# Performance work log

Measured on AMD Instinct MI355X. Metric: run time of the kernel, lower is better.

Reference implementation:

```python
import jax, jax.numpy as jnp
import numpy as np

BITS = 4
PACK = 32 // BITS            # 8 nibbles per int32
IN, OUT = 4096, 4096
NNZ = 75008


def setup_inputs() -> dict:
    key = jax.random.key(0)
    ks = jax.random.split(key, 7)
    x = jax.random.normal(ks[0], (4, 2048, IN), jnp.float32)
    # packed 4-bit indices: any int32 bit pattern is valid after masking
    qweight = jax.random.randint(ks[1], (IN // PACK, OUT), 0, 2147483647, jnp.int32)
    lookup_table = jax.random.normal(ks[2], (OUT, 2 ** BITS), jnp.float32)
    bias = jax.random.normal(ks[3], (OUT,), jnp.float32)
    rows = jnp.sort(jax.random.randint(ks[4], (OUT + 1,), 0, NNZ, jnp.int32))
    outlier_rows = rows.at[0].set(0).at[-1].set(NNZ)  # valid CSR crow
    outlier_cols = jax.random.randint(ks[5], (NNZ,), 0, IN, jnp.int32)
    outlier_vals = jax.random.normal(ks[6], (NNZ,), jnp.float32)
    return {
        'x': x,
        'lookup_table': lookup_table,
        'bias': bias,
        'outlier_vals': outlier_vals,
        'qweight': qweight,
        'outlier_rows': outlier_rows,
        'outlier_cols': outlier_cols,
    }


def _dequant_weight(qweight, lookup_table):
    # unpack 8 4-bit indices per int32 along the packed-infeatures axis
    shifts = (jnp.arange(PACK, dtype=jnp.int32) * BITS)
    idx = ((qweight[:, None, :] >> shifts[None, :, None]) & 0xF)  # [IN//8, 8, OUT]
    idx = idx.reshape(IN, OUT)                                     # [IN, OUT]
    # per-output-channel LUT gather: W[o, i] = lut[o, idx[i, o]]
    return jnp.take_along_axis(lookup_table, idx.T, axis=1)       # [OUT, IN]


def reference(x, lookup_table, bias, outlier_vals, qweight, outlier_rows, outlier_cols):
    W = _dequant_weight(qweight, lookup_table)
    # CSR outlier correction: scatter-add sparse values into the dense weight
    row_ids = jnp.clip(
        jnp.searchsorted(outlier_rows, jnp.arange(NNZ, dtype=jnp.int32), side='right') - 1,
        0, OUT - 1)
    W = W.at[row_ids, outlier_cols].add(outlier_vals)
    x2 = x.reshape(-1, IN)
    y = x2 @ W.T + bias                                            # [B, OUT]
    return y.reshape(x.shape[:-1] + (OUT,))
```

## Files before the change

### kernel.cpp

```cpp
#include <hip/hip_runtime.h>
#include <stdint.h>

#define IN_F  4096
#define OUT_F 4096

typedef unsigned short u16;
typedef __attribute__((ext_vector_type(8))) short bf16x8;
typedef __attribute__((ext_vector_type(4))) float f32x4;

__device__ __forceinline__ u16 f2bf(float f) {
    union { float f; unsigned u; } c; c.f = f;
    unsigned u = c.u;
    return (u16)((u + 0x7FFFu + ((u >> 16) & 1u)) >> 16);
}
__device__ __forceinline__ float bf2f(u16 h) {
    union { unsigned u; float f; } c; c.u = ((unsigned)h) << 16;
    return c.f;
}

__device__ __forceinline__ void load_lds16(const void* g, void* l) {
    unsigned loff = (unsigned)(uintptr_t)l;
    loff = (unsigned)__builtin_amdgcn_readfirstlane((int)loff);
    __builtin_amdgcn_global_load_lds(
        (const __attribute__((address_space(1))) void*)(uintptr_t)g,
        (__attribute__((address_space(3))) void*)(uintptr_t)loff,
        16, 0, 0);
}

#define DQ_O 64
#define DQ_I 256

__global__ __launch_bounds__(256) void dequant_k(const int* __restrict__ qw,
                                                 const float* __restrict__ lut,
                                                 const int* __restrict__ rows,
                                                 const int* __restrict__ cols,
                                                 const float* __restrict__ vals,
                                                 u16* __restrict__ W) {
    __shared__ __align__(16) u16 sW[DQ_O * DQ_I];
    __shared__ u16 slut[DQ_O * 18];

    const int tid = threadIdx.x;
    const int o0 = blockIdx.y * DQ_O;
    const int i0 = blockIdx.x * DQ_I;
    const int p0 = i0 >> 3;

    {
        const int idx = tid * 4;
        const float4 v = *(const float4*)(lut + (size_t)o0 * 16 + idx);
        u16* d = slut + (idx >> 4) * 18 + (idx & 15);
        d[0] = f2bf(v.x); d[1] = f2bf(v.y); d[2] = f2bf(v.z); d[3] = f2bf(v.w);
    }
    __syncthreads();

    const int o_l = tid & 63;
    const int swz = o_l & 31;
#pragma unroll
    for (int it = 0; it < 8; ++it) {
        const int p = (tid >> 6) + it * 4;
        const unsigned w = (unsigned)qw[(size_t)(p0 + p) * OUT_F + (o0 + o_l)];
        union { u16 h[8]; uint4 v; } u;
#pragma unroll
        for (int j = 0; j < 8; ++j)
            u.h[j] = slut[o_l * 18 + ((w >> (4 * j)) & 15u)];
        *(uint4*)(sW + o_l * DQ_I + ((p ^ swz) << 3)) = u.v;
    }
    __syncthreads();

    if (tid < DQ_O) {
        const int s = rows[o0 + tid], e = rows[o0 + tid + 1];
        for (int k = s; k < e; ++k) {
            const unsigned j = (unsigned)(cols[k] - i0);
            if (j < DQ_I) {
                u16* p16 = sW + tid * DQ_I + (((j >> 3) ^ swz) << 3) + (j & 7);
                *p16 = f2bf(bf2f(*p16) + vals[k]);
            }
        }
    }
    __syncthreads();

    const int ch = tid & 31;
#pragma unroll
    for (int it = 0; it < 8; ++it) {
        const int r = (tid >> 5) + it * 8;
        *(uint4*)(W + (size_t)(o0 + r) * IN_F + i0 + ch * 8) =
            *(const uint4*)(sW + r * DQ_I + ((ch ^ (r & 31)) << 3));
    }
}

__global__ __launch_bounds__(256) void cvtx_k(const float4* __restrict__ x,
                                              u16* __restrict__ xb) {
    const size_t i = (size_t)blockIdx.x * 256 + threadIdx.x;
    const float4 a = x[2 * i];
    const float4 b = x[2 * i + 1];
    union { u16 h[8]; uint4 v; } u;
    u.h[0] = f2bf(a.x); u.h[1] = f2bf(a.y); u.h[2] = f2bf(a.z); u.h[3] = f2bf(a.w);
    u.h[4] = f2bf(b.x); u.h[5] = f2bf(b.y); u.h[6] = f2bf(b.z); u.h[7] = f2bf(b.w);
    *(uint4*)(xb + i * 8) = u.v;
}

#define BM 128
#define BN 128
#define BK 32
#define GK 4096

__global__ __launch_bounds__(256) void gemm_k(const u16* __restrict__ A,
                                              const u16* __restrict__ B,
                                              const float* __restrict__ bias,
                                              float* __restrict__ C,
                                              int M, int N) {
    __shared__ __align__(16) u16 sA[BM * BK];
    __shared__ __align__(16) u16 sB[BN * BK];

    const int tid  = threadIdx.x;
    const int wave = tid >> 6;
    const int lane = tid & 63;
    const int bm = blockIdx.y * BM;
    const int bn = blockIdx.x * BN;

    const int srow = wave * 16 + (lane >> 2);
    const int scol = (lane & 3) * 8;

    const u16* ga0 = A + (size_t)(bm + srow) * GK + scol;
    const u16* ga1 = ga0 + (size_t)64 * GK;
    const u16* gb0 = B + (size_t)(bn + srow) * GK + scol;
    const u16* gb1 = gb0 + (size_t)64 * GK;

    u16* la0 = sA + wave * 512;
    u16* la1 = la0 + 2048;
    u16* lb0 = sB + wave * 512;
    u16* lb1 = lb0 + 2048;

    const int frow = lane & 15;
    const int fk   = (lane >> 4) * 8;

    const int wm = (wave >> 1) * 64;
    const int wn = (wave & 1) * 64;

    f32x4 acc[4][4] = {};

    for (int k0 = 0; k0 < GK; k0 += BK) {
        __syncthreads();
        load_lds16(ga0 + k0, la0);
        load_lds16(ga1 + k0, la1);
        load_lds16(gb0 + k0, lb0);
        load_lds16(gb1 + k0, lb1);
        __syncthreads();

        bf16x8 af[4], bfr[4];
#pragma unroll
        for (int t = 0; t < 4; ++t) {
            af[t]  = *(const bf16x8*)(sA + (wm + t * 16 + frow) * BK + fk);
            bfr[t] = *(const bf16x8*)(sB + (wn + t * 16 + frow) * BK + fk);
        }
#pragma unroll
        for (int i = 0; i < 4; ++i)
#pragma unroll
            for (int j = 0; j < 4; ++j)
                acc[i][j] = __builtin_amdgcn_mfma_f32_16x16x32_bf16(
                    af[i], bfr[j], acc[i][j], 0, 0, 0);
    }

    const int cm = bm + wm;
    const int cn = bn + wn;
#pragma unroll
    for (int j = 0; j < 4; ++j) {
        const int col = cn + j * 16 + (lane & 15);
        const float bv = bias[col];
#pragma unroll
        for (int i = 0; i < 4; ++i) {
            const int r0 = cm + i * 16 + (lane >> 4) * 4;
#pragma unroll
            for (int r = 0; r < 4; ++r)
                C[(size_t)(r0 + r) * N + col] = acc[i][j][r] + bv;
        }
    }
}

extern "C" void kernel_launch(void* const* d_in, const int* in_sizes, int n_in,
                              void* d_out, int out_size, void* d_ws, size_t ws_size,
                              hipStream_t stream) {
    (void)n_in; (void)out_size; (void)ws_size;
    const float* x     = (const float*)d_in[0];
    const float* lut   = (const float*)d_in[1];
    const float* bias  = (const float*)d_in[2];
    const float* ovals = (const float*)d_in[3];
    const int*   qw    = (const int*)d_in[4];
    const int*   orows = (const int*)d_in[5];
    const int*   ocols = (const int*)d_in[6];
    float* y = (float*)d_out;

    const int M = in_sizes[0] / IN_F;

    u16* W  = (u16*)d_ws;
    u16* xb = (u16*)((char*)d_ws + (size_t)OUT_F * IN_F * 2);

    dim3 dq_grid(IN_F / DQ_I, OUT_F / DQ_O);
    dequant_k<<<dq_grid, 256, 0, stream>>>(qw, lut, orows, ocols, ovals, W);
    cvtx_k<<<(size_t)M * IN_F / 8 / 256, 256, 0, stream>>>((const float4*)x, xb);
    dim3 grid(OUT_F / BN, M / BM);
    gemm_k<<<grid, 256, 0, stream>>>(xb, W, bias, y, M, OUT_F);
}
```

Before: 562.7 us.

## Fuse fp32-to-bf16 activation conversion into GEMM A-tile loads

Drops the separate cvtx kernel that converted x to a bf16 workspace copy. The GEMM now streams fp32 activation tiles straight into LDS with a rotated column layout, then packs them to bf16 with a perm instruction while building MFMA fragments. This removes one full read and write pass over the activations and one kernel launch. In exchange, each GEMM block moves twice as many A bytes through global/L2 and LDS per k-step, and the rounding changes from round-to-nearest-even to round-half-up.

```diff
diff --git a/kernel.cpp b/kernel.cpp
--- a/kernel.cpp
+++ b/kernel.cpp
@@ -16,6 +16,10 @@
 __device__ __forceinline__ float bf2f(u16 h) {
     union { unsigned u; float f; } c; c.u = ((unsigned)h) << 16;
     return c.f;
+}
+__device__ __forceinline__ unsigned pkbf(float lo, float hi) {
+    union { float f; unsigned u; } a, b; a.f = lo; b.f = hi;
+    return __builtin_amdgcn_perm(b.u + 0x8000u, a.u + 0x8000u, 0x07060302u);
 }
 
 __device__ __forceinline__ void load_lds16(const void* g, void* l) {
@@ -87,29 +91,18 @@
     }
 }
 
-__global__ __launch_bounds__(256) void cvtx_k(const float4* __restrict__ x,
-                                              u16* __restrict__ xb) {
-    const size_t i = (size_t)blockIdx.x * 256 + threadIdx.x;
-    const float4 a = x[2 * i];
-    const float4 b = x[2 * i + 1];
-    union { u16 h[8]; uint4 v; } u;
-    u.h[0] = f2bf(a.x); u.h[1] = f2bf(a.y); u.h[2] = f2bf(a.z); u.h[3] = f2bf(a.w);
-    u.h[4] = f2bf(b.x); u.h[5] = f2bf(b.y); u.h[6] = f2bf(b.z); u.h[7] = f2bf(b.w);
-    *(uint4*)(xb + i * 8) = u.v;
-}
-
 #define BM 128
 #define BN 128
 #define BK 32
 #define GK 4096
 
-__global__ __launch_bounds__(256) void gemm_k(const u16* __restrict__ A,
+__global__ __launch_bounds__(256) void gemm_k(const float* __restrict__ X,
                                               const u16* __restrict__ B,
                                               const float* __restrict__ bias,
                                               float* __restrict__ C,
                                               int M, int N) {
-    __shared__ __align__(16) u16 sA[BM * BK];
-    __shared__ __align__(16) u16 sB[BN * BK];
+    __shared__ __align__(16) float sA[BM * BK];
+    __shared__ __align__(16) u16   sB[BN * BK];
 
     const int tid  = threadIdx.x;
     const int wave = tid >> 6;
@@ -117,21 +110,24 @@
     const int bm = blockIdx.y * BM;
     const int bn = blockIdx.x * BN;
 
+    const int ar = lane >> 3;
+    const int ac = lane & 7;
+    const int akoff = (((ac - ar) & 7) << 2);
+    const float* gA = X + (size_t)(bm + wave * 8 + ar) * GK + akoff;
+    float* laA = sA + (wave * 8) * BK;
+
     const int srow = wave * 16 + (lane >> 2);
     const int scol = (lane & 3) * 8;
-
-    const u16* ga0 = A + (size_t)(bm + srow) * GK + scol;
-    const u16* ga1 = ga0 + (size_t)64 * GK;
     const u16* gb0 = B + (size_t)(bn + srow) * GK + scol;
     const u16* gb1 = gb0 + (size_t)64 * GK;
-
-    u16* la0 = sA + wave * 512;
-    u16* la1 = la0 + 2048;
     u16* lb0 = sB + wave * 512;
     u16* lb1 = lb0 + 2048;
 
     const int frow = lane & 15;
-    const int fk   = (lane >> 4) * 8;
+    const int q    = lane >> 4;
+    const int fkB  = q * 8;
+    const int s0   = ((q * 8) + ((frow & 7) << 2)) & 31;
+    const int s1   = (s0 + 4) & 31;
 
     const int wm = (wave >> 1) * 64;
     const int wn = (wave & 1) * 64;
@@ -140,24 +136,32 @@
 
     for (int k0 = 0; k0 < GK; k0 += BK) {
         __syncthreads();
-        load_lds16(ga0 + k0, la0);
-        load_lds16(ga1 + k0, la1);
+#pragma unroll
+        for (int it = 0; it < 4; ++it)
+            load_lds16(gA + k0 + (size_t)it * 32 * GK, laA + it * 32 * BK);
         load_lds16(gb0 + k0, lb0);
         load_lds16(gb1 + k0, lb1);
         __syncthreads();
 
-        bf16x8 af[4], bfr[4];
+        bf16x8 bfr[4];
+        union { bf16x8 v; unsigned u[4]; } af[4];
 #pragma unroll
         for (int t = 0; t < 4; ++t) {
-            af[t]  = *(const bf16x8*)(sA + (wm + t * 16 + frow) * BK + fk);
-            bfr[t] = *(const bf16x8*)(sB + (wn + t * 16 + frow) * BK + fk);
+            const float* pa = sA + (wm + t * 16 + frow) * BK;
+            const float4 f0 = *(const float4*)(pa + s0);
+            const float4 f1 = *(const float4*)(pa + s1);
+            af[t].u[0] = pkbf(f0.x, f0.y);
+            af[t].u[1] = pkbf(f0.z, f0.w);
+            af[t].u[2] = pkbf(f1.x, f1.y);
+            af[t].u[3] = pkbf(f1.z, f1.w);
+            bfr[t] = *(const bf16x8*)(sB + (wn + t * 16 + frow) * BK + fkB);
         }
 #pragma unroll
         for (int i = 0; i < 4; ++i)
 #pragma unroll
             for (int j = 0; j < 4; ++j)
                 acc[i][j] = __builtin_amdgcn_mfma_f32_16x16x32_bf16(
-                    af[i], bfr[j], acc[i][j], 0, 0, 0);
+                    af[i].v, bfr[j], acc[i][j], 0, 0, 0);
     }
 
     const int cm = bm + wm;
@@ -191,12 +195,10 @@
 
     const int M = in_sizes[0] / IN_F;
 
-    u16* W  = (u16*)d_ws;
-    u16* xb = (u16*)((char*)d_ws + (size_t)OUT_F * IN_F * 2);
+    u16* W = (u16*)d_ws;
 
     dim3 dq_grid(IN_F / DQ_I, OUT_F / DQ_O);
     dequant_k<<<dq_grid, 256, 0, stream>>>(qw, lut, orows, ocols, ovals, W);
-    cvtx_k<<<(size_t)M * IN_F / 8 / 256, 256, 0, stream>>>((const float4*)x, xb);
     dim3 grid(OUT_F / BN, M / BM);
-    gemm_k<<<grid, 256, 0, stream>>>(xb, W, bias, y, M, OUT_F);
-}
+    gemm_k<<<grid, 256, 0, stream>>>(x, W, bias, y, M, OUT_F);
+}
```

New measurement: 677.4 us. 20.4% more time.
